# Optimization experiments

Measured on AMD Instinct MI355X. Metric: run time of the kernel, lower is better.

## Reference

```python
import jax, jax.numpy as jnp
import numpy as np

NEG_INF = -1000000.0  # matches the original's -1e6 masking constant


def setup_inputs() -> dict:
    key = jax.random.key(0)
    ks = jax.random.split(key, 7)
    B, S, A, Q, D = 32, 2048, 1024, 1024, 1024  # batch, src len, attend_dim, query_dim, att_dim
    return {
        "input": jax.random.normal(ks[0], (B, 1, Q), dtype=jnp.float32),
        "context": jax.random.normal(ks[1], (B, S, A), dtype=jnp.float32),
        "W_pre": jax.random.normal(ks[2], (D, A), dtype=jnp.float32) * 0.02,
        "b_pre": jax.random.normal(ks[3], (D,), dtype=jnp.float32) * 0.02,
        "W_q": jax.random.normal(ks[4], (D, Q), dtype=jnp.float32) * 0.02,
        "v": jax.random.normal(ks[5], (D,), dtype=jnp.float32) * 0.02,
        "mask": jax.random.randint(ks[6], (B, 1, S), 0, 2, dtype=jnp.int32),
    }


def reference(input, context, W_pre, b_pre, W_q, v, mask):
    # precompute = linear_pre(context): [B, S, D]
    precompute = jnp.einsum("bsa,da->bsd", context, W_pre) + b_pre
    # targetT = linear_q(input): [B, 1, D]; repeat over S via broadcast
    targetT = jnp.einsum("bqc,dc->bqd", input, W_q)
    tmp = jnp.tanh(precompute + targetT)                 # [B, S, D]
    energy = jnp.einsum("bsd,d->bs", tmp, v)             # linear_v -> [B, S]
    # mask: positions where mask == 0 get -1e6 (energy*(1-m) + m*(-1e6), m = (mask==0))
    masked_out = (mask[:, 0, :] == 0)
    energy = jnp.where(masked_out, NEG_INF, energy)
    score = jax.nn.softmax(energy, axis=1)               # softmax over S
    score_m = score[:, None, :]                          # [B, 1, S]
    weightedContext = jnp.einsum("bqs,bsa->bqa", score_m, context)  # [B, 1, A]
    return weightedContext, score_m, precompute
```

## Files before the change

kernel.cpp:

```cpp
#include <hip/hip_runtime.h>

#define NEG_INF_VAL -1000000.0f

typedef short s16x8 __attribute__((ext_vector_type(8)));
typedef float f32x4 __attribute__((ext_vector_type(4)));

__device__ __forceinline__ unsigned int bf16_rne(float f) {
  unsigned int u = __float_as_uint(f);
  return (u + 0x7fffu + ((u >> 16) & 1u)) >> 16;
}
__device__ __forceinline__ unsigned int pack_bf2(float a, float b) {
  return bf16_rne(a) | (bf16_rne(b) << 16);
}

__device__ __forceinline__ float fast_tanh(float x) {
  float xc = fminf(fmaxf(x, -15.f), 15.f);
  float t = __expf(2.f * xc);
  return __fdividef(t - 1.f, t + 1.f);
}

__global__ __launch_bounds__(256) void convert_bf16_kernel(
    const float* __restrict__ src, unsigned short* __restrict__ dst, long n) {
  long i = ((long)blockIdx.x * blockDim.x + threadIdx.x) * 8;
  long stride = (long)gridDim.x * blockDim.x * 8;
  for (; i < n; i += stride) {
    float4 f0 = *(const float4*)(src + i);
    float4 f1 = *(const float4*)(src + i + 4);
    uint4 o;
    o.x = pack_bf2(f0.x, f0.y);
    o.y = pack_bf2(f0.z, f0.w);
    o.z = pack_bf2(f1.x, f1.y);
    o.w = pack_bf2(f1.z, f1.w);
    *(uint4*)(dst + i) = o;
  }
}

__global__ __launch_bounds__(256) void targetT_kernel(
    const float* __restrict__ input, const float* __restrict__ Wq,
    float* __restrict__ tT) {
  int d0 = blockIdx.x * 8;
  int t = threadIdx.x;
  int b = t >> 3, dl = t & 7;
  __shared__ float in_s[32][32];
  __shared__ float wq_s[8][32];
  float acc = 0.f;
  for (int q0 = 0; q0 < 1024; q0 += 32) {
    int r = t >> 3, c = (t & 7) * 4;
    *(float4*)&in_s[r][c] = *(const float4*)&input[r * 1024 + q0 + c];
    wq_s[t >> 5][t & 31] = Wq[(long)(d0 + (t >> 5)) * 1024 + q0 + (t & 31)];
    __syncthreads();
#pragma unroll
    for (int qq = 0; qq < 32; ++qq)
      acc += in_s[b][qq] * wq_s[dl][qq];
    __syncthreads();
  }
  tT[b * 1024 + d0 + dl] = acc;
}

__device__ __forceinline__ void load_lds16(const void* g, void* l) {
  __builtin_amdgcn_global_load_lds(
      (const __attribute__((address_space(1))) void*)g,
      (__attribute__((address_space(3))) void*)l, 16, 0, 0);
}

__global__ __launch_bounds__(512, 2) void gemm_energy_kernel(
    const unsigned short* __restrict__ A,
    const unsigned short* __restrict__ B,
    const float* __restrict__ b_pre,
    const float* __restrict__ tT,
    const float* __restrict__ vvec,
    float* __restrict__ Cout,
    float* __restrict__ epart) {
  const int K = 1024;
  int lin = blockIdx.x;
  int w = (lin & 7) * 128 + (lin >> 3);
  int nt = w & 3;
  int mt = w >> 2;
  int m0 = mt * 256, n0 = nt * 256;
  int tid = threadIdx.x;
  int lane = tid & 63, wid = tid >> 6;
  int wr = wid >> 2, wc = wid & 3;
  int r = lane & 15, g = lane >> 4;

  __shared__ unsigned short sMem[2][2][256 * 64];

  f32x4 acc[8][4] = {};

  int rl = tid >> 3;
  int swcol = ((tid & 7) ^ (rl & 7)) * 8;
  const unsigned short* ap[4];
  const unsigned short* bp[4];
#pragma unroll
  for (int j = 0; j < 4; ++j) {
    ap[j] = A + (long)(m0 + j * 64 + rl) * K + swcol;
    bp[j] = B + (long)(n0 + j * 64 + rl) * K + swcol;
  }

  auto stage = [&](int buf) {
    char* la = (char*)&sMem[buf][0][0] + wid * 1024;
    char* lb = (char*)&sMem[buf][1][0] + wid * 1024;
#pragma unroll
    for (int j = 0; j < 4; ++j) { load_lds16(ap[j], la + j * 8192); ap[j] += 64; }
#pragma unroll
    for (int j = 0; j < 4; ++j) { load_lds16(bp[j], lb + j * 8192); bp[j] += 64; }
  };

  auto compute = [&](int buf) {
    const unsigned short* bA = &sMem[buf][0][0];
    const unsigned short* bB = &sMem[buf][1][0];
#pragma unroll
    for (int kk = 0; kk < 2; ++kk) {
      int slot = ((kk * 4 + g) ^ (r & 7)) * 8;
      s16x8 af[8], bfv[4];
#pragma unroll
      for (int i = 0; i < 8; ++i)
        af[i] = *(const s16x8*)(bA + (wr * 128 + i * 16 + r) * 64 + slot);
#pragma unroll
      for (int j = 0; j < 4; ++j)
        bfv[j] = *(const s16x8*)(bB + (wc * 64 + j * 16 + r) * 64 + slot);
      __builtin_amdgcn_s_setprio(1);
#pragma unroll
      for (int i = 0; i < 8; ++i)
#pragma unroll
        for (int j = 0; j < 4; ++j)
          acc[i][j] = __builtin_amdgcn_mfma_f32_16x16x32_bf16(af[i], bfv[j], acc[i][j], 0, 0, 0);
      __builtin_amdgcn_s_setprio(0);
    }
  };

  stage(0);
  stage(1);
  asm volatile("s_waitcnt vmcnt(8)" ::: "memory");
  __builtin_amdgcn_s_barrier();

#pragma unroll 1
  for (int it = 0; it < 7; ++it) {
    compute(0);
    asm volatile("s_waitcnt lgkmcnt(0)" ::: "memory");
    __builtin_amdgcn_s_barrier();
    stage(0);
    asm volatile("s_waitcnt vmcnt(8)" ::: "memory");
    __builtin_amdgcn_s_barrier();

    compute(1);
    asm volatile("s_waitcnt lgkmcnt(0)" ::: "memory");
    __builtin_amdgcn_s_barrier();
    stage(1);
    asm volatile("s_waitcnt vmcnt(8)" ::: "memory");
    __builtin_amdgcn_s_barrier();
  }
  compute(0);
  asm volatile("s_waitcnt lgkmcnt(0)" ::: "memory");
  __builtin_amdgcn_s_barrier();
  asm volatile("s_waitcnt vmcnt(0)" ::: "memory");
  __builtin_amdgcn_s_barrier();
  compute(1);

  int b = m0 >> 11;
  float bias[4], tv[4], vv[4];
#pragma unroll
  for (int j = 0; j < 4; ++j) {
    int d = n0 + wc * 64 + j * 16 + r;
    bias[j] = b_pre[d];
    tv[j] = tT[b * 1024 + d];
    vv[j] = vvec[d];
  }
#pragma unroll
  for (int i = 0; i < 8; ++i) {
#pragma unroll
    for (int q = 0; q < 4; ++q) {
      int m = m0 + wr * 128 + i * 16 + g * 4 + q;
      float e = 0.f;
#pragma unroll
      for (int j = 0; j < 4; ++j) {
        float val = acc[i][j][q] + bias[j];
        Cout[(long)m * 1024 + n0 + wc * 64 + j * 16 + r] = val;
        e += fast_tanh(val + tv[j]) * vv[j];
      }
      e += __shfl_xor(e, 1);
      e += __shfl_xor(e, 2);
      e += __shfl_xor(e, 4);
      e += __shfl_xor(e, 8);
      if (r == 0) epart[(long)m * 16 + nt * 4 + wc] = e;
    }
  }
}

__global__ __launch_bounds__(256) void softmax_kernel(
    const float* __restrict__ epart, const int* __restrict__ mask,
    float* __restrict__ score) {
  int b = blockIdx.x;
  int t = threadIdx.x;
  __shared__ float red[256];
  float ev[8];
  float mx = -3.4e38f;
#pragma unroll
  for (int ii = 0; ii < 8; ++ii) {
    int s = ii * 256 + t;
    long m = (long)b * 2048 + s;
    const float4* p = (const float4*)(epart + m * 16);
    float4 p0 = p[0], p1 = p[1], p2 = p[2], p3 = p[3];
    float e = p0.x + p0.y + p0.z + p0.w + p1.x + p1.y + p1.z + p1.w
            + p2.x + p2.y + p2.z + p2.w + p3.x + p3.y + p3.z + p3.w;
    if (mask[b * 2048 + s] == 0) e = NEG_INF_VAL;
    ev[ii] = e;
    mx = fmaxf(mx, e);
  }
  red[t] = mx; __syncthreads();
  for (int off = 128; off > 0; off >>= 1) {
    if (t < off) red[t] = fmaxf(red[t], red[t + off]);
    __syncthreads();
  }
  mx = red[0];
  __syncthreads();
  float sum = 0.f;
#pragma unroll
  for (int ii = 0; ii < 8; ++ii) { ev[ii] = __expf(ev[ii] - mx); sum += ev[ii]; }
  red[t] = sum; __syncthreads();
  for (int off = 128; off > 0; off >>= 1) {
    if (t < off) red[t] += red[t + off];
    __syncthreads();
  }
  float inv = 1.f / red[0];
#pragma unroll
  for (int ii = 0; ii < 8; ++ii)
    score[b * 2048 + ii * 256 + t] = ev[ii] * inv;
}

__global__ __launch_bounds__(256) void wc_partial_kernel(
    const unsigned short* __restrict__ ctx, const float* __restrict__ score,
    float* __restrict__ part) {
  int b = blockIdx.x, sc = blockIdx.y;
  int t = threadIdx.x;
  __shared__ float ssc[64];
  if (t < 64) ssc[t] = score[b * 2048 + sc * 64 + t];
  __syncthreads();
  float acc0 = 0.f, acc1 = 0.f, acc2 = 0.f, acc3 = 0.f;
  const unsigned short* cp = ctx + ((long)b * 2048 + sc * 64) * 1024 + t * 4;
  for (int s = 0; s < 64; ++s) {
    uint2 pk = *(const uint2*)cp;
    cp += 1024;
    float wgt = ssc[s];
    acc0 += wgt * __uint_as_float(pk.x << 16);
    acc1 += wgt * __uint_as_float(pk.x & 0xffff0000u);
    acc2 += wgt * __uint_as_float(pk.y << 16);
    acc3 += wgt * __uint_as_float(pk.y & 0xffff0000u);
  }
  float* pp = part + ((long)(b * 32 + sc)) * 1024 + t * 4;
  pp[0] = acc0; pp[1] = acc1; pp[2] = acc2; pp[3] = acc3;
}

__global__ __launch_bounds__(256) void wc_reduce_kernel(
    const float* __restrict__ part, float* __restrict__ wc) {
  int id = blockIdx.x * 256 + threadIdx.x;
  int b = id >> 10, a = id & 1023;
  float s = 0.f;
#pragma unroll
  for (int scn = 0; scn < 32; ++scn)
    s += part[((long)(b * 32 + scn)) * 1024 + a];
  wc[id] = s;
}

extern "C" void kernel_launch(void* const* d_in, const int* in_sizes, int n_in,
                              void* d_out, int out_size, void* d_ws, size_t ws_size,
                              hipStream_t stream) {
  const float* input   = (const float*)d_in[0];
  const float* context = (const float*)d_in[1];
  const float* W_pre   = (const float*)d_in[2];
  const float* b_pre   = (const float*)d_in[3];
  const float* W_q     = (const float*)d_in[4];
  const float* v       = (const float*)d_in[5];
  const int*   mask    = (const int*)d_in[6];

  float* out       = (float*)d_out;
  float* out_wc    = out;
  float* out_score = out + 32768;
  float* out_pre   = out + 98304;

  const size_t OFF_CTX   = 0;
  const size_t OFF_WPRE  = 134217728;
  const size_t OFF_TT    = 136314880;
  const size_t OFF_EPART = 136445952;
  const size_t OFF_WCP   = 140640256;
  const size_t WS_NEED   = 144834560;
  if (ws_size < WS_NEED) return;

  char* ws = (char*)d_ws;
  unsigned short* ctx_bf  = (unsigned short*)(ws + OFF_CTX);
  unsigned short* wpre_bf = (unsigned short*)(ws + OFF_WPRE);
  float* tT     = (float*)(ws + OFF_TT);
  float* epart  = (float*)(ws + OFF_EPART);
  float* wcpart = (float*)(ws + OFF_WCP);

  convert_bf16_kernel<<<2048, 256, 0, stream>>>(context, ctx_bf, 64LL * 1024 * 1024);
  convert_bf16_kernel<<<256, 256, 0, stream>>>(W_pre, wpre_bf, 1024LL * 1024);
  targetT_kernel<<<128, 256, 0, stream>>>(input, W_q, tT);
  gemm_energy_kernel<<<1024, 512, 0, stream>>>(ctx_bf, wpre_bf, b_pre, tT, v,
                                               out_pre, epart);
  softmax_kernel<<<32, 256, 0, stream>>>(epart, mask, out_score);
  dim3 g5(32, 32);
  wc_partial_kernel<<<g5, 256, 0, stream>>>(ctx_bf, out_score, wcpart);
  wc_reduce_kernel<<<128, 256, 0, stream>>>(wcpart, out_wc);
}
```

Measured before the change: 363.5 us.

## Interleave half-tile LDS staging with MFMA phases in the GEMM main loop

Restructures the bf16 GEMM main loop into eight fine-grained phases per two K-tiles. Each phase loads a quarter of the A fragments, optionally the B fragments, issues one half-matrix global-to-LDS stage, then runs 16 MFMAs. The LDS layout is split into 32-wide K halves with a new XOR swizzle. The goal is to overlap global loads with compute more evenly and reduce register pressure from holding all fragments at once. In exchange there are many more barriers, and the clamped kt index issues redundant loads on the last iterations.

```diff
diff --git a/kernel.cpp b/kernel.cpp
--- a/kernel.cpp
+++ b/kernel.cpp
@@ -63,15 +63,48 @@
       (__attribute__((address_space(3))) void*)l, 16, 0, 0);
 }
 
+#define MFMA_ROW(QI, I, AF)                                                          \
+  acc[(QI)*4+(I)][0] = __builtin_amdgcn_mfma_f32_16x16x32_bf16(AF, bf0, acc[(QI)*4+(I)][0], 0, 0, 0); \
+  acc[(QI)*4+(I)][1] = __builtin_amdgcn_mfma_f32_16x16x32_bf16(AF, bf1, acc[(QI)*4+(I)][1], 0, 0, 0); \
+  acc[(QI)*4+(I)][2] = __builtin_amdgcn_mfma_f32_16x16x32_bf16(AF, bf2, acc[(QI)*4+(I)][2], 0, 0, 0); \
+  acc[(QI)*4+(I)][3] = __builtin_amdgcn_mfma_f32_16x16x32_bf16(AF, bf3, acc[(QI)*4+(I)][3], 0, 0, 0);
+
+#define PHASE(BUF, QI, KK, LOADB, SB, SM, SK, SKT, VM)                               \
+  {                                                                                  \
+    const unsigned short* bA = &sMem[BUF][0][KK][0];                                 \
+    s16x8 af0 = *(const s16x8*)(bA + (wr*128 + ((QI)*4+0)*16 + r)*32 + physoff);     \
+    s16x8 af1 = *(const s16x8*)(bA + (wr*128 + ((QI)*4+1)*16 + r)*32 + physoff);     \
+    s16x8 af2 = *(const s16x8*)(bA + (wr*128 + ((QI)*4+2)*16 + r)*32 + physoff);     \
+    s16x8 af3 = *(const s16x8*)(bA + (wr*128 + ((QI)*4+3)*16 + r)*32 + physoff);     \
+    if (LOADB) {                                                                     \
+      const unsigned short* bB = &sMem[BUF][1][KK][0];                               \
+      bf0 = *(const s16x8*)(bB + (wc*64 +  0 + r)*32 + physoff);                     \
+      bf1 = *(const s16x8*)(bB + (wc*64 + 16 + r)*32 + physoff);                     \
+      bf2 = *(const s16x8*)(bB + (wc*64 + 32 + r)*32 + physoff);                     \
+      bf3 = *(const s16x8*)(bB + (wc*64 + 48 + r)*32 + physoff);                     \
+    }                                                                                \
+    stage_half(SB, SM, SK, SKT);                                                     \
+    __builtin_amdgcn_s_barrier();                                                    \
+    asm volatile("s_waitcnt lgkmcnt(0)" ::: "memory");                               \
+    __builtin_amdgcn_sched_barrier(0);                                               \
+    __builtin_amdgcn_s_setprio(1);                                                   \
+    MFMA_ROW(QI, 0, af0)                                                             \
+    MFMA_ROW(QI, 1, af1)                                                             \
+    MFMA_ROW(QI, 2, af2)                                                             \
+    MFMA_ROW(QI, 3, af3)                                                             \
+    __builtin_amdgcn_s_setprio(0);                                                   \
+    if (VM) asm volatile("s_waitcnt vmcnt(8)" ::: "memory");                         \
+    __builtin_amdgcn_s_barrier();                                                    \
+  }
+
 __global__ __launch_bounds__(512, 2) void gemm_energy_kernel(
     const unsigned short* __restrict__ A,
-    const unsigned short* __restrict__ B,
+    const unsigned short* __restrict__ Bm,
     const float* __restrict__ b_pre,
     const float* __restrict__ tT,
     const float* __restrict__ vvec,
     float* __restrict__ Cout,
     float* __restrict__ epart) {
-  const int K = 1024;
   int lin = blockIdx.x;
   int w = (lin & 7) * 128 + (lin >> 3);
   int nt = w & 3;
@@ -82,79 +115,44 @@
   int wr = wid >> 2, wc = wid & 3;
   int r = lane & 15, g = lane >> 4;
 
-  __shared__ unsigned short sMem[2][2][256 * 64];
+  __shared__ unsigned short sMem[2][2][2][256 * 32];
 
   f32x4 acc[8][4] = {};
-
-  int rl = tid >> 3;
-  int swcol = ((tid & 7) ^ (rl & 7)) * 8;
-  const unsigned short* ap[4];
-  const unsigned short* bp[4];
-#pragma unroll
-  for (int j = 0; j < 4; ++j) {
-    ap[j] = A + (long)(m0 + j * 64 + rl) * K + swcol;
-    bp[j] = B + (long)(n0 + j * 64 + rl) * K + swcol;
-  }
-
-  auto stage = [&](int buf) {
-    char* la = (char*)&sMem[buf][0][0] + wid * 1024;
-    char* lb = (char*)&sMem[buf][1][0] + wid * 1024;
-#pragma unroll
-    for (int j = 0; j < 4; ++j) { load_lds16(ap[j], la + j * 8192); ap[j] += 64; }
-#pragma unroll
-    for (int j = 0; j < 4; ++j) { load_lds16(bp[j], lb + j * 8192); bp[j] += 64; }
+  s16x8 bf0, bf1, bf2, bf3;
+
+  int physoff = (g ^ ((r >> 1) & 3)) * 8;
+
+  int srow = tid >> 2;
+  int slog8 = ((tid & 3) ^ ((tid >> 3) & 3)) * 8;
+  const unsigned short* Abase = A + (long)(m0 + srow) * 1024 + slog8;
+  const unsigned short* Bbase = Bm + (long)(n0 + srow) * 1024 + slog8;
+
+  auto stage_half = [&](int buf, int mat, int kk, int kt) {
+    int kc = kt > 15 ? 15 : kt;
+    long koff = kc * 64 + kk * 32;
+    const unsigned short* gp = (mat ? Bbase : Abase) + koff;
+    char* lb = (char*)&sMem[buf][mat][kk][0] + wid * 1024;
+    load_lds16(gp, lb);
+    load_lds16(gp + 128L * 1024, lb + 8192);
   };
 
-  auto compute = [&](int buf) {
-    const unsigned short* bA = &sMem[buf][0][0];
-    const unsigned short* bB = &sMem[buf][1][0];
-#pragma unroll
-    for (int kk = 0; kk < 2; ++kk) {
-      int slot = ((kk * 4 + g) ^ (r & 7)) * 8;
-      s16x8 af[8], bfv[4];
-#pragma unroll
-      for (int i = 0; i < 8; ++i)
-        af[i] = *(const s16x8*)(bA + (wr * 128 + i * 16 + r) * 64 + slot);
-#pragma unroll
-      for (int j = 0; j < 4; ++j)
-        bfv[j] = *(const s16x8*)(bB + (wc * 64 + j * 16 + r) * 64 + slot);
-      __builtin_amdgcn_s_setprio(1);
-#pragma unroll
-      for (int i = 0; i < 8; ++i)
-#pragma unroll
-        for (int j = 0; j < 4; ++j)
-          acc[i][j] = __builtin_amdgcn_mfma_f32_16x16x32_bf16(af[i], bfv[j], acc[i][j], 0, 0, 0);
-      __builtin_amdgcn_s_setprio(0);
-    }
-  };
-
-  stage(0);
-  stage(1);
+  stage_half(0, 0, 0, 0); stage_half(0, 1, 0, 0);
+  stage_half(0, 0, 1, 0); stage_half(0, 1, 1, 0);
+  stage_half(1, 0, 0, 1); stage_half(1, 1, 0, 1);
   asm volatile("s_waitcnt vmcnt(8)" ::: "memory");
   __builtin_amdgcn_s_barrier();
 
 #pragma unroll 1
-  for (int it = 0; it < 7; ++it) {
-    compute(0);
-    asm volatile("s_waitcnt lgkmcnt(0)" ::: "memory");
-    __builtin_amdgcn_s_barrier();
-    stage(0);
-    asm volatile("s_waitcnt vmcnt(8)" ::: "memory");
-    __builtin_amdgcn_s_barrier();
-
-    compute(1);
-    asm volatile("s_waitcnt lgkmcnt(0)" ::: "memory");
-    __builtin_amdgcn_s_barrier();
-    stage(1);
-    asm volatile("s_waitcnt vmcnt(8)" ::: "memory");
-    __builtin_amdgcn_s_barrier();
-  }
-  compute(0);
-  asm volatile("s_waitcnt lgkmcnt(0)" ::: "memory");
-  __builtin_amdgcn_s_barrier();
-  asm volatile("s_waitcnt vmcnt(0)" ::: "memory");
-  __builtin_amdgcn_s_barrier();
-  compute(1);
+  for (int t0 = 0; t0 < 16; t0 += 2) {
+    PHASE(0, 0, 0, 1, 1, 0, 1, t0 + 1, 0)
+    PHASE(0, 1, 0, 0, 1, 1, 1, t0 + 1, 1)
+    PHASE(0, 0, 1, 1, 0, 0, 0, t0 + 2, 0)
+    PHASE(0, 1, 1, 0, 0, 1, 0, t0 + 2, 1)
+    PHASE(1, 0, 0, 1, 0, 0, 1, t0 + 2, 0)
+    PHASE(1, 1, 0, 0, 0, 1, 1, t0 + 2, 1)
+    PHASE(1, 0, 1, 1, 1, 0, 0, t0 + 3, 0)
+    PHASE(1, 1, 1, 0, 1, 1, 0, t0 + 3, 1)
+  }
 
   int b = m0 >> 11;
   float bias[4], tv[4], vv[4];
```

Result: faster. 340.8 us (-6.2%).
